# Kernel optimization log

Hardware: AMD Instinct MI355X
Metric: run time of the kernel (lower is better)

## Reference

```python
import jax, jax.numpy as jnp
import numpy as np

N = 100000      # nodes
E = 1_000_000   # edges (avg degree ~10)
D_IN = 64
HID = 64
N_CLS = 32


def setup_inputs() -> dict:
    key = jax.random.key(0)
    ks = jax.random.split(key, 9)
    x = jax.random.normal(ks[0], (N, D_IN), dtype=jnp.float32)
    edge_index = jax.random.randint(ks[1], (2, E), 0, N, dtype=jnp.int32)
    s_in = 1.0 / np.sqrt(D_IN)
    s_h = 1.0 / np.sqrt(HID)
    W1 = jax.random.normal(ks[2], (D_IN, HID), dtype=jnp.float32) * s_in
    b1 = jnp.zeros((HID,), dtype=jnp.float32)
    W2 = jax.random.normal(ks[3], (HID, HID), dtype=jnp.float32) * s_h
    b2 = jnp.zeros((HID,), dtype=jnp.float32)
    Wl = jax.random.normal(ks[4], (HID, N_CLS), dtype=jnp.float32) * s_h
    bl = jnp.zeros((N_CLS,), dtype=jnp.float32)
    return {"x": x, "edge_index": edge_index,
            "W1": W1, "b1": b1, "W2": W2, "b2": b2, "Wl": Wl, "bl": bl}


def reference(x, edge_index, W1, b1, W2, b2, Wl, bl):
    # GCNConv default: add self-loops, symmetric normalization D^-1/2 (A+I) D^-1/2
    loop = jnp.arange(N, dtype=edge_index.dtype)
    src = jnp.concatenate([edge_index[0], loop])  # [E+N]
    dst = jnp.concatenate([edge_index[1], loop])  # [E+N]

    deg = jax.ops.segment_sum(jnp.ones_like(dst, dtype=jnp.float32), dst,
                              num_segments=N)              # [N]
    dinv = jnp.where(deg > 0, jax.lax.rsqrt(deg), 0.0)      # D^-1/2
    norm = dinv[src] * dinv[dst]                            # [E+N]

    def gcn_conv(h, W, b):
        h = h @ W                                           # [N, F_out]
        msg = h[src] * norm[:, None]                        # gather + scale
        return jax.ops.segment_sum(msg, dst, num_segments=N) + b

    h = jax.nn.relu(gcn_conv(x, W1, b1))
    h = jax.nn.relu(gcn_conv(h, W2, b2))
    return h @ Wl + bl
```

## Files before the change

kernel.cpp:

```cpp
#include <hip/hip_runtime.h>
#include <hip/hip_fp16.h>
#include <math.h>


#define TPB    256
#define TPB1   1024
#define EBLKS  256
#define BSH    7
#define BNODES (1 << BSH)
#define CAPSH  11
#define CAP    (1 << CAPSH)

__global__ __launch_bounds__(TPB1)
void k_scatter(const int* __restrict__ src, const int* __restrict__ dst,
               int* __restrict__ gcnt, int* __restrict__ ebuf,
               int E, int CH, int NBC) {
    __shared__ int h[1024];
    int tid = threadIdx.x, b = blockIdx.x;
    h[tid] = 0;
    __syncthreads();
    int beg = b * CH, end = min(E, beg + CH);
    if (beg < end) {
        int nfull = (end - beg) & ~3;
        for (int i = beg + tid * 4; i < beg + nfull; i += TPB1 * 4) {
            int4 d = *(const int4*)&dst[i];
            atomicAdd(&h[d.x >> BSH], 1);
            atomicAdd(&h[d.y >> BSH], 1);
            atomicAdd(&h[d.z >> BSH], 1);
            atomicAdd(&h[d.w >> BSH], 1);
        }
        if (tid < (end - beg) - nfull)
            atomicAdd(&h[dst[beg + nfull + tid] >> BSH], 1);
    }
    __syncthreads();
    for (int c = tid; c < NBC; c += TPB1) {
        int n = h[c];
        int base = (n > 0) ? atomicAdd(&gcnt[c], n) : 0;
        h[c] = (c << CAPSH) + base;
    }
    __syncthreads();
    if (beg >= end) return;
    int nfull = (end - beg) & ~3;
    for (int i = beg + tid * 4; i < beg + nfull; i += TPB1 * 4) {
        int4 s4 = *(const int4*)&src[i];
        int4 d4 = *(const int4*)&dst[i];
        int p0 = atomicAdd(&h[d4.x >> BSH], 1);
        int p1 = atomicAdd(&h[d4.y >> BSH], 1);
        int p2 = atomicAdd(&h[d4.z >> BSH], 1);
        int p3 = atomicAdd(&h[d4.w >> BSH], 1);
        ebuf[p0] = (s4.x << BSH) | (d4.x & (BNODES - 1));
        ebuf[p1] = (s4.y << BSH) | (d4.y & (BNODES - 1));
        ebuf[p2] = (s4.z << BSH) | (d4.z & (BNODES - 1));
        ebuf[p3] = (s4.w << BSH) | (d4.w & (BNODES - 1));
    }
    if (tid < (end - beg) - nfull) {
        int i = beg + nfull + tid;
        int d = dst[i];
        int p = atomicAdd(&h[d >> BSH], 1);
        ebuf[p] = (src[i] << BSH) | (d & (BNODES - 1));
    }
}

__global__ __launch_bounds__(TPB)
void k_p2f(const int* __restrict__ ebuf, const int* __restrict__ gcnt,
           int* __restrict__ row_ptr, int* __restrict__ row_end,
           float* __restrict__ dinv, int* __restrict__ colw,
           int N, int NBC) {
    __shared__ int cnt[BNODES];
    __shared__ int ofs[BNODES];
    __shared__ int s1[TPB];
    int tid = threadIdx.x, c = blockIdx.x;
    int beg = c << CAPSH;
    int end = beg + gcnt[c];
    if (tid < BNODES) cnt[tid] = 0;
    __syncthreads();
    for (int i = beg + tid; i < end; i += TPB)
        atomicAdd(&cnt[ebuf[i] & (BNODES - 1)], 1);
    __syncthreads();
    int a  = (tid < BNODES) ? cnt[tid] : 0;
    int ap = (a + 3) & ~3;
    s1[tid] = ap;
    __syncthreads();
    for (int off = 1; off < TPB; off <<= 1) {
        int x = (tid >= off) ? s1[tid - off] : 0;
        __syncthreads();
        s1[tid] += x;
        __syncthreads();
    }
    int ex = s1[tid] - ap;
    if (tid < BNODES) {
        int node = (c << BSH) + tid;
        ofs[tid] = beg + ex;
        if (node < N) {
            row_ptr[node] = beg + ex;
            row_end[node] = beg + ex + a;
            dinv[node]    = rsqrtf((float)(a + 1));
        }
        cnt[tid] = 0;
    }
    __syncthreads();
    for (int i0 = beg + tid; i0 < end; i0 += TPB * 4) {
        int sv[4], dl[4], pos[4];
        int have = 0;
#pragma unroll
        for (int k = 0; k < 4; ++k) {
            int i = i0 + k * TPB;
            if (i < end) {
                int e = ebuf[i];
                sv[k] = e >> BSH;
                dl[k] = e & (BNODES - 1);
                have = k + 1;
            }
        }
#pragma unroll
        for (int k = 0; k < 4; ++k) {
            if (k < have) {
                int r  = atomicAdd(&cnt[dl[k]], 1);
                pos[k] = ofs[dl[k]] + r;
            }
        }
#pragma unroll
        for (int k = 0; k < 4; ++k)
            if (k < have) colw[pos[k]] = sv[k];
    }
    __syncthreads();
    if (tid < BNODES) {
        int aa  = cnt[tid];
        int app = (aa + 3) & ~3;
        int o   = ofs[tid];
        for (int j = aa; j < app; ++j) colw[o + j] = N;
    }
}

__launch_bounds__(256)
__global__ void k_mm(const float* __restrict__ in, const float* __restrict__ W,
                     const float* __restrict__ dinv,
                     __half* __restrict__ out, int n) {
    __shared__ float in_s[64 * 68];
    __shared__ float w_s[64 * 64];

    const int tid  = threadIdx.x;
    const int row0 = blockIdx.x * 64;

    for (int i4 = tid; i4 < (64 * 64) / 4; i4 += 256)
        ((float4*)w_s)[i4] = ((const float4*)W)[i4];

    for (int idx = tid; idx < 64 * 16; idx += 256) {
        int r  = idx >> 4;
        int c4 = idx & 15;
        float4 v;
        if (row0 + r < n)
            v = *(const float4*)(in + (size_t)(row0 + r) * 64 + c4 * 4);
        else
            v = make_float4(0.f, 0.f, 0.f, 0.f);
        *(float4*)&in_s[r * 68 + c4 * 4] = v;
    }
    __syncthreads();

    constexpr int CPT = 4;
    const int tx = tid & 15;
    const int ty = tid >> 4;

    float acc[4][CPT];
#pragma unroll
    for (int r = 0; r < 4; ++r)
#pragma unroll
        for (int c = 0; c < CPT; ++c) acc[r][c] = 0.f;

#pragma unroll 4
    for (int k = 0; k < 64; ++k) {
        float b[CPT];
#pragma unroll
        for (int c = 0; c < CPT; ++c) b[c] = w_s[k * 64 + tx * CPT + c];
#pragma unroll
        for (int r = 0; r < 4; ++r) {
            float a = in_s[(ty * 4 + r) * 68 + k];
#pragma unroll
            for (int c = 0; c < CPT; ++c) acc[r][c] = fmaf(a, b[c], acc[r][c]);
        }
    }

#pragma unroll
    for (int r = 0; r < 4; ++r) {
        int row = row0 + ty * 4 + r;
        if (row >= n) continue;
        float dd = dinv[row];
        __half2 p0 = __floats2half2_rn(acc[r][0] * dd, acc[r][1] * dd);
        __half2 p1 = __floats2half2_rn(acc[r][2] * dd, acc[r][3] * dd);
        uint2 u = make_uint2(*(unsigned*)&p0, *(unsigned*)&p1);
        *(uint2*)(out + (size_t)row * 64 + tx * 4) = u;
    }
    if (blockIdx.x == 0 && tid < 16)
        *(uint2*)(out + (size_t)n * 64 + tid * 4) = make_uint2(0u, 0u);
}

__global__ __launch_bounds__(256)
void k_gather_mm(const int* __restrict__ row_ptr, const int* __restrict__ row_end,
                 const int* __restrict__ colw,
                 const float* __restrict__ dinv, const float* __restrict__ bias,
                 const __half* __restrict__ t, const float* __restrict__ W2,
                 __half* __restrict__ t2, int N) {
    __shared__ float  w_s[64 * 64];
    __shared__ __half aggs[32][72];

    int tid = threadIdx.x;
    for (int i4 = tid; i4 < (64 * 64) / 4; i4 += 256)
        ((float4*)w_s)[i4] = ((const float4*)W2)[i4];

    int wv   = tid >> 6;
    int lane = tid & 63;
    int g = lane >> 3;
    int p = lane & 7;
    int slot = tid >> 3;
    int d = blockIdx.x * 32 + wv * 8 + g;

    int beg = 0, end = 0;
    if (d < N) { beg = row_ptr[d]; end = row_end[d]; }

    float acc[8];
#pragma unroll
    for (int k = 0; k < 8; ++k) acc[k] = 0.f;

    for (int e = beg; e < end; e += 4) {
        int4 v = *(const int4*)&colw[e];
        uint4 a0 = *(const uint4*)(t + (size_t)v.x * 64 + p * 8);
        uint4 a1 = *(const uint4*)(t + (size_t)v.y * 64 + p * 8);
        uint4 a2 = *(const uint4*)(t + (size_t)v.z * 64 + p * 8);
        uint4 a3 = *(const uint4*)(t + (size_t)v.w * 64 + p * 8);
        float2 f;
        f = __half22float2(*(__half2*)&a0.x); acc[0] += f.x; acc[1] += f.y;
        f = __half22float2(*(__half2*)&a0.y); acc[2] += f.x; acc[3] += f.y;
        f = __half22float2(*(__half2*)&a0.z); acc[4] += f.x; acc[5] += f.y;
        f = __half22float2(*(__half2*)&a0.w); acc[6] += f.x; acc[7] += f.y;
        f = __half22float2(*(__half2*)&a1.x); acc[0] += f.x; acc[1] += f.y;
        f = __half22float2(*(__half2*)&a1.y); acc[2] += f.x; acc[3] += f.y;
        f = __half22float2(*(__half2*)&a1.z); acc[4] += f.x; acc[5] += f.y;
        f = __half22float2(*(__half2*)&a1.w); acc[6] += f.x; acc[7] += f.y;
        f = __half22float2(*(__half2*)&a2.x); acc[0] += f.x; acc[1] += f.y;
        f = __half22float2(*(__half2*)&a2.y); acc[2] += f.x; acc[3] += f.y;
        f = __half22float2(*(__half2*)&a2.z); acc[4] += f.x; acc[5] += f.y;
        f = __half22float2(*(__half2*)&a2.w); acc[6] += f.x; acc[7] += f.y;
        f = __half22float2(*(__half2*)&a3.x); acc[0] += f.x; acc[1] += f.y;
        f = __half22float2(*(__half2*)&a3.y); acc[2] += f.x; acc[3] += f.y;
        f = __half22float2(*(__half2*)&a3.z); acc[4] += f.x; acc[5] += f.y;
        f = __half22float2(*(__half2*)&a3.w); acc[6] += f.x; acc[7] += f.y;
    }

    if (d < N) {
        float dd = dinv[d];
        uint4 a = *(const uint4*)(t + (size_t)d * 64 + p * 8);
        float4 b0 = *(const float4*)&bias[p * 8];
        float4 b1 = *(const float4*)&bias[p * 8 + 4];
        float2 s0 = __half22float2(*(__half2*)&a.x);
        float2 s1 = __half22float2(*(__half2*)&a.y);
        float2 s2 = __half22float2(*(__half2*)&a.z);
        float2 s3 = __half22float2(*(__half2*)&a.w);
        float o0 = fmaxf(fmaf(dd, acc[0] + s0.x, b0.x), 0.f);
        float o1 = fmaxf(fmaf(dd, acc[1] + s0.y, b0.y), 0.f);
        float o2 = fmaxf(fmaf(dd, acc[2] + s1.x, b0.z), 0.f);
        float o3 = fmaxf(fmaf(dd, acc[3] + s1.y, b0.w), 0.f);
        float o4 = fmaxf(fmaf(dd, acc[4] + s2.x, b1.x), 0.f);
        float o5 = fmaxf(fmaf(dd, acc[5] + s2.y, b1.y), 0.f);
        float o6 = fmaxf(fmaf(dd, acc[6] + s3.x, b1.z), 0.f);
        float o7 = fmaxf(fmaf(dd, acc[7] + s3.y, b1.w), 0.f);
        __half2 h0 = __floats2half2_rn(o0, o1);
        __half2 h1 = __floats2half2_rn(o2, o3);
        __half2 h2 = __floats2half2_rn(o4, o5);
        __half2 h3 = __floats2half2_rn(o6, o7);
        *(uint4*)&aggs[slot][p * 8] = make_uint4(*(unsigned*)&h0, *(unsigned*)&h1,
                                                *(unsigned*)&h2, *(unsigned*)&h3);
    }
    __syncthreads();

    if (d < N) {
        float dd = dinv[d];
        float a0 = 0.f, a1 = 0.f, a2 = 0.f, a3 = 0.f;
        float a4 = 0.f, a5 = 0.f, a6 = 0.f, a7 = 0.f;
#pragma unroll
        for (int k0 = 0; k0 < 64; k0 += 8) {
            uint4 u = *(const uint4*)&aggs[slot][k0];
            float2 f0 = __half22float2(*(__half2*)&u.x);
            float2 f1 = __half22float2(*(__half2*)&u.y);
            float2 f2 = __half22float2(*(__half2*)&u.z);
            float2 f3 = __half22float2(*(__half2*)&u.w);
            float av[8] = {f0.x, f0.y, f1.x, f1.y, f2.x, f2.y, f3.x, f3.y};
#pragma unroll
            for (int j = 0; j < 8; ++j) {
                const float* wr = &w_s[(k0 + j) * 64 + p * 8];
                float4 w0 = *(const float4*)&wr[0];
                float4 w1 = *(const float4*)&wr[4];
                a0 = fmaf(av[j], w0.x, a0);
                a1 = fmaf(av[j], w0.y, a1);
                a2 = fmaf(av[j], w0.z, a2);
                a3 = fmaf(av[j], w0.w, a3);
                a4 = fmaf(av[j], w1.x, a4);
                a5 = fmaf(av[j], w1.y, a5);
                a6 = fmaf(av[j], w1.z, a6);
                a7 = fmaf(av[j], w1.w, a7);
            }
        }
        __half2 q0 = __floats2half2_rn(a0 * dd, a1 * dd);
        __half2 q1 = __floats2half2_rn(a2 * dd, a3 * dd);
        __half2 q2 = __floats2half2_rn(a4 * dd, a5 * dd);
        __half2 q3 = __floats2half2_rn(a6 * dd, a7 * dd);
        uint4 u = make_uint4(*(unsigned*)&q0, *(unsigned*)&q1,
                             *(unsigned*)&q2, *(unsigned*)&q3);
        *(uint4*)(t2 + (size_t)d * 64 + p * 8) = u;
    }
    if (blockIdx.x == 0 && tid < 16)
        *(uint2*)(t2 + (size_t)N * 64 + tid * 4) = make_uint2(0u, 0u);
}

__global__ __launch_bounds__(256)
void k_gather_head(const int* __restrict__ row_ptr, const int* __restrict__ row_end,
                   const int* __restrict__ colw,
                   const float* __restrict__ dinv, const float* __restrict__ bias,
                   const __half* __restrict__ t, const float* __restrict__ Wl,
                   const float* __restrict__ bl, float* __restrict__ out, int N) {
    __shared__ float wl_s[64 * 32];
    __shared__ float aggs[32][68];

    int tid  = threadIdx.x;
    for (int i4 = tid; i4 < (64 * 32) / 4; i4 += 256)
        ((float4*)wl_s)[i4] = ((const float4*)Wl)[i4];

    int wv   = tid >> 6;
    int lane = tid & 63;
    int g = lane >> 3;
    int p = lane & 7;
    int slot = tid >> 3;
    int d = blockIdx.x * 32 + wv * 8 + g;

    int beg = 0, end = 0;
    if (d < N) { beg = row_ptr[d]; end = row_end[d]; }

    float acc[8];
#pragma unroll
    for (int k = 0; k < 8; ++k) acc[k] = 0.f;

    for (int e = beg; e < end; e += 4) {
        int4 v = *(const int4*)&colw[e];
        uint4 a0 = *(const uint4*)(t + (size_t)v.x * 64 + p * 8);
        uint4 a1 = *(const uint4*)(t + (size_t)v.y * 64 + p * 8);
        uint4 a2 = *(const uint4*)(t + (size_t)v.z * 64 + p * 8);
        uint4 a3 = *(const uint4*)(t + (size_t)v.w * 64 + p * 8);
        float2 f;
        f = __half22float2(*(__half2*)&a0.x); acc[0] += f.x; acc[1] += f.y;
        f = __half22float2(*(__half2*)&a0.y); acc[2] += f.x; acc[3] += f.y;
        f = __half22float2(*(__half2*)&a0.z); acc[4] += f.x; acc[5] += f.y;
        f = __half22float2(*(__half2*)&a0.w); acc[6] += f.x; acc[7] += f.y;
        f = __half22float2(*(__half2*)&a1.x); acc[0] += f.x; acc[1] += f.y;
        f = __half22float2(*(__half2*)&a1.y); acc[2] += f.x; acc[3] += f.y;
        f = __half22float2(*(__half2*)&a1.z); acc[4] += f.x; acc[5] += f.y;
        f = __half22float2(*(__half2*)&a1.w); acc[6] += f.x; acc[7] += f.y;
        f = __half22float2(*(__half2*)&a2.x); acc[0] += f.x; acc[1] += f.y;
        f = __half22float2(*(__half2*)&a2.y); acc[2] += f.x; acc[3] += f.y;
        f = __half22float2(*(__half2*)&a2.z); acc[4] += f.x; acc[5] += f.y;
        f = __half22float2(*(__half2*)&a2.w); acc[6] += f.x; acc[7] += f.y;
        f = __half22float2(*(__half2*)&a3.x); acc[0] += f.x; acc[1] += f.y;
        f = __half22float2(*(__half2*)&a3.y); acc[2] += f.x; acc[3] += f.y;
        f = __half22float2(*(__half2*)&a3.z); acc[4] += f.x; acc[5] += f.y;
        f = __half22float2(*(__half2*)&a3.w); acc[6] += f.x; acc[7] += f.y;
    }

    if (d < N) {
        float dd = dinv[d];
        uint4 a = *(const uint4*)(t + (size_t)d * 64 + p * 8);
        float4 b0 = *(const float4*)&bias[p * 8];
        float4 b1 = *(const float4*)&bias[p * 8 + 4];
        float2 s0 = __half22float2(*(__half2*)&a.x);
        float2 s1 = __half22float2(*(__half2*)&a.y);
        float2 s2 = __half22float2(*(__half2*)&a.z);
        float2 s3 = __half22float2(*(__half2*)&a.w);
        float o0 = fmaxf(fmaf(dd, acc[0] + s0.x, b0.x), 0.f);
        float o1 = fmaxf(fmaf(dd, acc[1] + s0.y, b0.y), 0.f);
        float o2 = fmaxf(fmaf(dd, acc[2] + s1.x, b0.z), 0.f);
        float o3 = fmaxf(fmaf(dd, acc[3] + s1.y, b0.w), 0.f);
        float o4 = fmaxf(fmaf(dd, acc[4] + s2.x, b1.x), 0.f);
        float o5 = fmaxf(fmaf(dd, acc[5] + s2.y, b1.y), 0.f);
        float o6 = fmaxf(fmaf(dd, acc[6] + s3.x, b1.z), 0.f);
        float o7 = fmaxf(fmaf(dd, acc[7] + s3.y, b1.w), 0.f);
        *(float4*)&aggs[slot][p * 8]     = make_float4(o0, o1, o2, o3);
        *(float4*)&aggs[slot][p * 8 + 4] = make_float4(o4, o5, o6, o7);
    }
    __syncthreads();

    if (d < N) {
        float a0 = 0.f, a1 = 0.f, a2 = 0.f, a3 = 0.f;
#pragma unroll 8
        for (int k = 0; k < 64; ++k) {
            float av = aggs[slot][k];
            float4 w = ((const float4*)&wl_s[k * 32])[p];
            a0 = fmaf(av, w.x, a0);
            a1 = fmaf(av, w.y, a1);
            a2 = fmaf(av, w.z, a2);
            a3 = fmaf(av, w.w, a3);
        }
        float4 bb = *(const float4*)&bl[p * 4];
        *(float4*)&out[(size_t)d * 32 + p * 4] =
            make_float4(a0 + bb.x, a1 + bb.y, a2 + bb.z, a3 + bb.w);
    }
}

extern "C" void kernel_launch(void* const* d_in, const int* in_sizes, int n_in,
                              void* d_out, int out_size, void* d_ws, size_t ws_size,
                              hipStream_t stream) {
    const float* x  = (const float*)d_in[0];
    const int*   ei = (const int*)d_in[1];
    const float* W1 = (const float*)d_in[2];
    const float* b1 = (const float*)d_in[3];
    const float* W2 = (const float*)d_in[4];
    const float* b2 = (const float*)d_in[5];
    const float* Wl = (const float*)d_in[6];
    const float* bl = (const float*)d_in[7];
    float*       out = (float*)d_out;

    const int N = in_sizes[0] / 64;
    const int E = in_sizes[1] / 2;
    const int* srcp = ei;
    const int* dstp = ei + E;

    const int NBC = (N + BNODES - 1) / BNODES;
    const int CH  = (((E + EBLKS - 1) / EBLKS) + 3) & ~3;

    char*  ws  = (char*)d_ws;
    size_t off = 0;
    auto alloc = [&](size_t bytes) -> void* {
        void* p = (void*)(ws + off);
        off += (bytes + 255) & ~(size_t)255;
        return p;
    };
    int*    gcnt    = (int*)alloc((size_t)NBC * 4);
    int*    ebuf    = (int*)alloc((size_t)NBC * CAP * 4);
    int*    colw    = (int*)alloc((size_t)NBC * CAP * 4);
    int*    row_ptr = (int*)alloc((size_t)N * 4);
    int*    row_end = (int*)alloc((size_t)N * 4);
    float*  dinv    = (float*)alloc((size_t)N * 4);
    __half* t1      = (__half*)alloc((size_t)(N + 1) * 64 * 2);
    __half* t2      = (__half*)alloc((size_t)(N + 1) * 64 * 2);

    const int nb_mm = (N + 63) / 64;
    const int nb_g  = (N + 31) / 32;

    hipMemsetAsync(gcnt, 0, (size_t)NBC * 4, stream);
    k_scatter<<<EBLKS, TPB1, 0, stream>>>(srcp, dstp, gcnt, ebuf, E, CH, NBC);
    k_p2f    <<<NBC,   TPB,  0, stream>>>(ebuf, gcnt, row_ptr, row_end,
                                          dinv, colw, N, NBC);

    k_mm<<<nb_mm, 256, 0, stream>>>(x, W1, dinv, t1, N);

    k_gather_mm<<<nb_g, 256, 0, stream>>>(row_ptr, row_end, colw, dinv, b1,
                                          t1, W2, t2, N);

    k_gather_head<<<nb_g, 256, 0, stream>>>(row_ptr, row_end, colw, dinv, b2,
                                            t2, Wl, bl, out, N);
}
```

Before: 184.4 us.

## Split each node's edge gather across two 8-lane groups and use wave-shuffle scan

```diff
diff --git a/kernel.cpp b/kernel.cpp
--- a/kernel.cpp
+++ b/kernel.cpp
@@ -68,7 +68,7 @@
            int N, int NBC) {
     __shared__ int cnt[BNODES];
     __shared__ int ofs[BNODES];
-    __shared__ int s1[TPB];
+    __shared__ int w0sum;
     int tid = threadIdx.x, c = blockIdx.x;
     int beg = c << CAPSH;
     int end = beg + gcnt[c];
@@ -79,15 +79,15 @@
     __syncthreads();
     int a  = (tid < BNODES) ? cnt[tid] : 0;
     int ap = (a + 3) & ~3;
-    s1[tid] = ap;
-    __syncthreads();
-    for (int off = 1; off < TPB; off <<= 1) {
-        int x = (tid >= off) ? s1[tid - off] : 0;
-        __syncthreads();
-        s1[tid] += x;
-        __syncthreads();
-    }
-    int ex = s1[tid] - ap;
+    int v = ap;
+#pragma unroll
+    for (int off = 1; off < 64; off <<= 1) {
+        int x = __shfl_up(v, off);
+        if ((tid & 63) >= off) v += x;
+    }
+    if (tid == 63) w0sum = v;
+    __syncthreads();
+    int ex = (v - ap) + ((tid >= 64 && tid < BNODES) ? w0sum : 0);
     if (tid < BNODES) {
         int node = (c << BSH) + tid;
         ofs[tid] = beg + ex;
@@ -201,27 +201,29 @@
                  const __half* __restrict__ t, const float* __restrict__ W2,
                  __half* __restrict__ t2, int N) {
     __shared__ float  w_s[64 * 64];
-    __shared__ __half aggs[32][72];
+    __shared__ __half aggs[16][72];
 
     int tid = threadIdx.x;
     for (int i4 = tid; i4 < (64 * 64) / 4; i4 += 256)
         ((float4*)w_s)[i4] = ((const float4*)W2)[i4];
 
-    int wv   = tid >> 6;
-    int lane = tid & 63;
-    int g = lane >> 3;
-    int p = lane & 7;
-    int slot = tid >> 3;
-    int d = blockIdx.x * 32 + wv * 8 + g;
-
-    int beg = 0, end = 0;
-    if (d < N) { beg = row_ptr[d]; end = row_end[d]; }
+    const int p    = tid & 7;
+    const int h    = (tid >> 3) & 1;
+    const int slot = tid >> 4;
+    const int d    = blockIdx.x * 16 + slot;
+
+    int beg = 0, pe = 0;
+    if (d < N) {
+        beg = row_ptr[d];
+        int end = row_end[d];
+        pe  = beg + ((end - beg + 3) & ~3);
+    }
 
     float acc[8];
 #pragma unroll
     for (int k = 0; k < 8; ++k) acc[k] = 0.f;
 
-    for (int e = beg; e < end; e += 4) {
+    for (int e = beg + h * 4; e < pe; e += 8) {
         int4 v = *(const int4*)&colw[e];
         uint4 a0 = *(const uint4*)(t + (size_t)v.x * 64 + p * 8);
         uint4 a1 = *(const uint4*)(t + (size_t)v.y * 64 + p * 8);
@@ -245,8 +247,10 @@
         f = __half22float2(*(__half2*)&a3.z); acc[4] += f.x; acc[5] += f.y;
         f = __half22float2(*(__half2*)&a3.w); acc[6] += f.x; acc[7] += f.y;
     }
-
-    if (d < N) {
+#pragma unroll
+    for (int k = 0; k < 8; ++k) acc[k] += __shfl_xor(acc[k], 8);
+
+    if (d < N && h == 0) {
         float dd = dinv[d];
         uint4 a = *(const uint4*)(t + (size_t)d * 64 + p * 8);
         float4 b0 = *(const float4*)&bias[p * 8];
@@ -274,8 +278,8 @@
 
     if (d < N) {
         float dd = dinv[d];
+        const int q = tid & 15;
         float a0 = 0.f, a1 = 0.f, a2 = 0.f, a3 = 0.f;
-        float a4 = 0.f, a5 = 0.f, a6 = 0.f, a7 = 0.f;
 #pragma unroll
         for (int k0 = 0; k0 < 64; k0 += 8) {
             uint4 u = *(const uint4*)&aggs[slot][k0];
@@ -286,26 +290,17 @@
             float av[8] = {f0.x, f0.y, f1.x, f1.y, f2.x, f2.y, f3.x, f3.y};
 #pragma unroll
             for (int j = 0; j < 8; ++j) {
-                const float* wr = &w_s[(k0 + j) * 64 + p * 8];
-                float4 w0 = *(const float4*)&wr[0];
-                float4 w1 = *(const float4*)&wr[4];
-                a0 = fmaf(av[j], w0.x, a0);
-                a1 = fmaf(av[j], w0.y, a1);
-                a2 = fmaf(av[j], w0.z, a2);
-                a3 = fmaf(av[j], w0.w, a3);
-                a4 = fmaf(av[j], w1.x, a4);
-                a5 = fmaf(av[j], w1.y, a5);
-                a6 = fmaf(av[j], w1.z, a6);
-                a7 = fmaf(av[j], w1.w, a7);
+                float4 w = *(const float4*)&w_s[(k0 + j) * 64 + q * 4];
+                a0 = fmaf(av[j], w.x, a0);
+                a1 = fmaf(av[j], w.y, a1);
+                a2 = fmaf(av[j], w.z, a2);
+                a3 = fmaf(av[j], w.w, a3);
             }
         }
         __half2 q0 = __floats2half2_rn(a0 * dd, a1 * dd);
         __half2 q1 = __floats2half2_rn(a2 * dd, a3 * dd);
-        __half2 q2 = __floats2half2_rn(a4 * dd, a5 * dd);
-        __half2 q3 = __floats2half2_rn(a6 * dd, a7 * dd);
-        uint4 u = make_uint4(*(unsigned*)&q0, *(unsigned*)&q1,
-                             *(unsigned*)&q2, *(unsigned*)&q3);
-        *(uint4*)(t2 + (size_t)d * 64 + p * 8) = u;
+        uint2 u = make_uint2(*(unsigned*)&q0, *(unsigned*)&q1);
+        *(uint2*)(t2 + (size_t)d * 64 + q * 4) = u;
     }
     if (blockIdx.x == 0 && tid < 16)
         *(uint2*)(t2 + (size_t)N * 64 + tid * 4) = make_uint2(0u, 0u);
@@ -318,27 +313,29 @@
                    const __half* __restrict__ t, const float* __restrict__ Wl,
                    const float* __restrict__ bl, float* __restrict__ out, int N) {
     __shared__ float wl_s[64 * 32];
-    __shared__ float aggs[32][68];
+    __shared__ float aggs[16][68];
 
     int tid  = threadIdx.x;
     for (int i4 = tid; i4 < (64 * 32) / 4; i4 += 256)
         ((float4*)wl_s)[i4] = ((const float4*)Wl)[i4];
 
-    int wv   = tid >> 6;
-    int lane = tid & 63;
-    int g = lane >> 3;
-    int p = lane & 7;
-    int slot = tid >> 3;
-    int d = blockIdx.x * 32 + wv * 8 + g;
-
-    int beg = 0, end = 0;
-    if (d < N) { beg = row_ptr[d]; end = row_end[d]; }
+    const int p    = tid & 7;
+    const int h    = (tid >> 3) & 1;
+    const int slot = tid >> 4;
+    const int d    = blockIdx.x * 16 + slot;
+
+    int beg = 0, pe = 0;
+    if (d < N) {
+        beg = row_ptr[d];
+        int end = row_end[d];
+        pe  = beg + ((end - beg + 3) & ~3);
+    }
 
     float acc[8];
 #pragma unroll
     for (int k = 0; k < 8; ++k) acc[k] = 0.f;
 
-    for (int e = beg; e < end; e += 4) {
+    for (int e = beg + h * 4; e < pe; e += 8) {
         int4 v = *(const int4*)&colw[e];
         uint4 a0 = *(const uint4*)(t + (size_t)v.x * 64 + p * 8);
         uint4 a1 = *(const uint4*)(t + (size_t)v.y * 64 + p * 8);
@@ -362,8 +359,10 @@
         f = __half22float2(*(__half2*)&a3.z); acc[4] += f.x; acc[5] += f.y;
         f = __half22float2(*(__half2*)&a3.w); acc[6] += f.x; acc[7] += f.y;
     }
-
-    if (d < N) {
+#pragma unroll
+    for (int k = 0; k < 8; ++k) acc[k] += __shfl_xor(acc[k], 8);
+
+    if (d < N && h == 0) {
         float dd = dinv[d];
         uint4 a = *(const uint4*)(t + (size_t)d * 64 + p * 8);
         float4 b0 = *(const float4*)&bias[p * 8];
@@ -386,19 +385,17 @@
     __syncthreads();
 
     if (d < N) {
-        float a0 = 0.f, a1 = 0.f, a2 = 0.f, a3 = 0.f;
+        const int q = tid & 15;
+        float a0 = 0.f, a1 = 0.f;
 #pragma unroll 8
         for (int k = 0; k < 64; ++k) {
             float av = aggs[slot][k];
-            float4 w = ((const float4*)&wl_s[k * 32])[p];
+            float2 w = *(const float2*)&wl_s[k * 32 + q * 2];
             a0 = fmaf(av, w.x, a0);
             a1 = fmaf(av, w.y, a1);
-            a2 = fmaf(av, w.z, a2);
-            a3 = fmaf(av, w.w, a3);
-        }
-        float4 bb = *(const float4*)&bl[p * 4];
-        *(float4*)&out[(size_t)d * 32 + p * 4] =
-            make_float4(a0 + bb.x, a1 + bb.y, a2 + bb.z, a3 + bb.w);
+        }
+        float2 bb = *(const float2*)&bl[q * 2];
+        *(float2*)&out[(size_t)d * 32 + q * 2] = make_float2(a0 + bb.x, a1 + bb.y);
     }
 }
 
@@ -440,7 +437,7 @@
     __half* t2      = (__half*)alloc((size_t)(N + 1) * 64 * 2);
 
     const int nb_mm = (N + 63) / 64;
-    const int nb_g  = (N + 31) / 32;
+    const int nb_g  = (N + 15) / 16;
 
     hipMemsetAsync(gcnt, 0, (size_t)NBC * 4, stream);
     k_scatter<<<EBLKS, TPB1, 0, stream>>>(srcp, dstp, gcnt, ebuf, E, CH, NBC);
```

Result: no change. 183.0 us (-0.7%).
